# Kernel optimization log

Hardware: AMD Instinct MI355X
Metric: run time of the kernel (lower is better)

Reference implementation:

```python
import jax, jax.numpy as jnp
import numpy as np

L = 2          # n_layer
H = 8          # n_head
DM = 512       # d_model
DFF = 2048     # d_ff
DH = DM // H   # head dim (query_dimensions)
M = DH         # Favor n_dims random features
B, S = 1, 2048
EPS = 1e-6     # causal linear attention eps
LN_EPS = 1e-5  # torch LayerNorm default


def setup_inputs() -> dict:
    key = jax.random.key(0)
    ks = jax.random.split(key, 12)
    sc = 0.02
    d = {}
    d['x'] = jax.random.normal(ks[0], (B, S, DM), dtype=jnp.float32)
    for i, (n, shape) in enumerate([('Wq', (L, DM, DM)), ('Wk', (L, DM, DM)),
                                    ('Wv', (L, DM, DM)), ('Wo', (L, DM, DM)),
                                    ('W1', (L, DM, DFF)), ('W2', (L, DFF, DM))]):
        d[n] = jax.random.normal(ks[i + 1], shape, dtype=jnp.float32) * sc
    d['bq'] = jnp.zeros((L, DM), jnp.float32)
    d['bk'] = jnp.zeros((L, DM), jnp.float32)
    d['bv'] = jnp.zeros((L, DM), jnp.float32)
    d['bo'] = jnp.zeros((L, DM), jnp.float32)
    d['b1'] = jnp.zeros((L, DFF), jnp.float32)
    d['b2'] = jnp.zeros((L, DM), jnp.float32)
    d['g1'] = jnp.ones((L, DM), jnp.float32)
    d['be1'] = jnp.zeros((L, DM), jnp.float32)
    d['g2'] = jnp.ones((L, DM), jnp.float32)
    d['be2'] = jnp.zeros((L, DM), jnp.float32)
    # FAVOR+ random projection matrix per layer: [Dh, M]
    d['omega'] = jax.random.normal(ks[7], (L, DH, M), dtype=jnp.float32)
    return d


def _favor(x, omega):
    # x: [B,S,H,Dh]; softmax_temp = 1/sqrt(Dh) applied as x * sqrt(temp)
    xs = x * (DH ** -0.25)
    nrm = jnp.sum(xs * xs, axis=-1, keepdims=True)       # [B,S,H,1]
    u = jnp.einsum('bshd,dm->bshm', xs, omega)           # [B,S,H,M]
    return jnp.exp(u - 0.5 * nrm) * (M ** -0.5)


def _ln(x, g, b):
    mu = jnp.mean(x, -1, keepdims=True)
    var = jnp.mean((x - mu) ** 2, -1, keepdims=True)
    return (x - mu) * jax.lax.rsqrt(var + LN_EPS) * g + b


def _forward(x, Wq, bq, Wk, bk, Wv, bv, Wo, bo, omega,
             W1, b1, W2, b2, g1, be1, g2, be2):
    out = x
    for l in range(L):
        q = (out @ Wq[l] + bq[l]).reshape(B, S, H, DH)
        k = (out @ Wk[l] + bk[l]).reshape(B, S, H, DH)
        v = (out @ Wv[l] + bv[l]).reshape(B, S, H, DH)
        pq = _favor(q, omega[l])
        pk = _favor(k, omega[l])
        # causal linear attention: running sums of phi(k) v^T and phi(k)
        kv = jnp.cumsum(jnp.einsum('bshm,bshd->bshmd', pk, v), axis=1)  # [B,S,H,M,Dh]
        num = jnp.einsum('bshm,bshmd->bshd', pq, kv)
        den = jnp.einsum('bshm,bshm->bsh', pq, jnp.cumsum(pk, axis=1)) + EPS
        a = (num / den[..., None]).reshape(B, S, DM)
        # post-norm encoder layer (fast-transformers TransformerEncoderLayer)
        out = out + (a @ Wo[l] + bo[l])
        out = _ln(out, g1[l], be1[l])
        y = jax.nn.relu(out @ W1[l] + b1[l]) @ W2[l] + b2[l]
        out = _ln(out + y, g2[l], be2[l])
    return out


def reference(x, Wq, bq, Wk, bk, Wv, bv, Wo, bo, omega,
              W1, b1, W2, b2, g1, be1, g2, be2):
    return _forward(x, Wq, bq, Wk, bk, Wv, bv, Wo, bo, omega,
                    W1, b1, W2, b2, g1, be1, g2, be2)
```

## Files before the change

kernel.cpp:

```cpp
#include <hip/hip_runtime.h>
#include <hip/hip_bf16.h>

#define S_  2048
#define DM_ 512
#define H_  8
#define DH_ 64
#define MF_ 64
#define DFF_ 2048
#define L_  2
#define CT_ 64
#define NC_ (S_ / CT_)
#define EPS_ 1e-6f
#define LN_EPS_ 1e-5f

typedef unsigned short ushortT;
typedef unsigned int u32;
typedef float f4 __attribute__((ext_vector_type(4)));
typedef short s8 __attribute__((ext_vector_type(8)));
typedef u32 u32x2 __attribute__((ext_vector_type(2)));

__device__ __forceinline__ ushortT f2b(float f) {
  union { float f; unsigned u; } v; v.f = f;
  unsigned r = v.u + 0x7fffu + ((v.u >> 16) & 1u);
  return (ushortT)(r >> 16);
}
__device__ __forceinline__ float bu2f(ushortT h) {
  union { unsigned u; float f; } v; v.u = ((unsigned)h) << 16; return v.f;
}
__device__ __forceinline__ u32 pk2(float a, float b) {
  return (u32)f2b(a) | ((u32)f2b(b) << 16);
}

__global__ __launch_bounds__(256) void copy_in(const float* __restrict__ x,
                                               float* __restrict__ cur,
                                               ushortT* __restrict__ curb) {
  int i = blockIdx.x * 256 + threadIdx.x;
  float v = x[i];
  cur[i] = v;
  curb[i] = f2b(v);
}

struct P4 { const float* p[4]; };
__global__ __launch_bounds__(256) void tcast(P4 srcs, int perLayer, int nper,
                                             ushortT* __restrict__ dstb,
                                             size_t layerStride, size_t wStride,
                                             int K, int N) {
  const int z = blockIdx.z;
  const int widx = (nper == 4) ? (z & 3) : 0;
  const int l = (nper == 4) ? (z >> 2) : z;
  const float* src = srcs.p[widx] + (size_t)l * perLayer;
  ushortT* dst = dstb + (size_t)l * layerStride + (size_t)widx * wStride;
  __shared__ ushortT tile[32][33];
  const int t = threadIdx.x;
  const int c = t & 31, r0 = t >> 5;
  const int n0 = blockIdx.x * 32, k0 = blockIdx.y * 32;
#pragma unroll
  for (int i = 0; i < 4; ++i) {
    int r = r0 + 8 * i;
    tile[r][c] = f2b(src[(size_t)(k0 + r) * N + n0 + c]);
  }
  __syncthreads();
#pragma unroll
  for (int i = 0; i < 4; ++i) {
    int r = r0 + 8 * i;
    dst[(size_t)(n0 + r) * K + k0 + c] = tile[c][r];
  }
}

template<bool RELU, bool HAS_RES, bool OUT_BF16>
__global__ __launch_bounds__(256) void mgemm(
    const ushortT* __restrict__ A, const ushortT* __restrict__ Wt,
    const float* __restrict__ bq_, const float* __restrict__ bk_,
    const float* __restrict__ bv_, const float* __restrict__ Res,
    float* __restrict__ Cf, ushortT* __restrict__ Cb, int K, int N) {
  __shared__ ushortT sA[2][2048];
  __shared__ ushortT sB[2][2048];
  const int t = threadIdx.x;
  const int w = t >> 6, l = t & 63;
  const int wm = w >> 1, wn = w & 1;
  const int n0 = blockIdx.x * 64, m0 = blockIdx.y * 64;
  const int z = blockIdx.z;
  const ushortT* Wz = Wt + (size_t)z * K * N;
  const float* bias = (z == 0) ? bq_ : (z == 1 ? bk_ : bv_);

  const int rs = w * 16 + (l >> 2);
  const int qs = (l & 3) ^ ((rs >> 1) & 3);
  const ushortT* gA = A  + (size_t)(m0 + rs) * K + qs * 8;
  const ushortT* gB = Wz + (size_t)(n0 + rs) * K + qs * 8;

  const int Ra = wm * 32 + (l & 15);
  const int Rb = wn * 32 + (l & 15);
  const int qq = l >> 4;
  const int aoff = (Ra * 4 + (qq ^ ((Ra >> 1) & 3))) * 8;
  const int boff = (Rb * 4 + (qq ^ ((Rb >> 1) & 3))) * 8;

  f4 acc[2][2];
#pragma unroll
  for (int i = 0; i < 2; ++i)
#pragma unroll
    for (int j = 0; j < 2; ++j) acc[i][j] = (f4){0.f, 0.f, 0.f, 0.f};

  auto stage = [&](int buf, int ko) {
    __builtin_amdgcn_global_load_lds(
        (const __attribute__((address_space(1))) void*)(gA + ko),
        (__attribute__((address_space(3))) void*)(&sA[buf][w * 512]), 16, 0, 0);
    __builtin_amdgcn_global_load_lds(
        (const __attribute__((address_space(1))) void*)(gB + ko),
        (__attribute__((address_space(3))) void*)(&sB[buf][w * 512]), 16, 0, 0);
  };

  stage(0, 0);
  const int nk = K >> 5;
  for (int ks = 0; ks < nk; ++ks) {
    __syncthreads();
    if (ks + 1 < nk) stage((ks + 1) & 1, (ks + 1) * 32);
    const ushortT* pa = sA[ks & 1];
    const ushortT* pb = sB[ks & 1];
    s8 a0 = *(const s8*)(pa + aoff);
    s8 a1 = *(const s8*)(pa + aoff + 512);
    s8 b0 = *(const s8*)(pb + boff);
    s8 b1 = *(const s8*)(pb + boff + 512);
    acc[0][0] = __builtin_amdgcn_mfma_f32_16x16x32_bf16(a0, b0, acc[0][0], 0, 0, 0);
    acc[0][1] = __builtin_amdgcn_mfma_f32_16x16x32_bf16(a0, b1, acc[0][1], 0, 0, 0);
    acc[1][0] = __builtin_amdgcn_mfma_f32_16x16x32_bf16(a1, b0, acc[1][0], 0, 0, 0);
    acc[1][1] = __builtin_amdgcn_mfma_f32_16x16x32_bf16(a1, b1, acc[1][1], 0, 0, 0);
  }

  const size_t outz = (size_t)z * S_ * N;
  const int colb = n0 + wn * 32 + (l & 15);
  const int rowb = m0 + wm * 32 + ((l >> 4) << 2);
#pragma unroll
  for (int mt = 0; mt < 2; ++mt) {
#pragma unroll
    for (int nt = 0; nt < 2; ++nt) {
      const int c = colb + nt * 16;
      const float bv = bias[c];
#pragma unroll
      for (int r = 0; r < 4; ++r) {
        const int rr = rowb + mt * 16 + r;
        float v = acc[mt][nt][r] + bv;
        if (HAS_RES) v += Res[(size_t)rr * N + c];
        if (RELU) v = fmaxf(v, 0.f);
        if (OUT_BF16) Cb[outz + (size_t)rr * N + c] = f2b(v);
        else          Cf[outz + (size_t)rr * N + c] = v;
      }
    }
  }
}

__global__ __launch_bounds__(256) void mgemm_part(
    const ushortT* __restrict__ A, const ushortT* __restrict__ Wt,
    float* __restrict__ PS, int K, int N, int KS) {
  __shared__ ushortT sA[2][2048];
  __shared__ ushortT sB[2][2048];
  const int t = threadIdx.x;
  const int w = t >> 6, l = t & 63;
  const int wm = w >> 1, wn = w & 1;
  const int n0 = blockIdx.x * 64, m0 = blockIdx.y * 64;
  const int z = blockIdx.z;

  const int rs = w * 16 + (l >> 2);
  const int qs = (l & 3) ^ ((rs >> 1) & 3);
  const ushortT* gA = A  + (size_t)(m0 + rs) * K + z * KS + qs * 8;
  const ushortT* gB = Wt + (size_t)(n0 + rs) * K + z * KS + qs * 8;

  const int Ra = wm * 32 + (l & 15);
  const int Rb = wn * 32 + (l & 15);
  const int qq = l >> 4;
  const int aoff = (Ra * 4 + (qq ^ ((Ra >> 1) & 3))) * 8;
  const int boff = (Rb * 4 + (qq ^ ((Rb >> 1) & 3))) * 8;

  f4 acc[2][2];
#pragma unroll
  for (int i = 0; i < 2; ++i)
#pragma unroll
    for (int j = 0; j < 2; ++j) acc[i][j] = (f4){0.f, 0.f, 0.f, 0.f};

  auto stage = [&](int buf, int ko) {
    __builtin_amdgcn_global_load_lds(
        (const __attribute__((address_space(1))) void*)(gA + ko),
        (__attribute__((address_space(3))) void*)(&sA[buf][w * 512]), 16, 0, 0);
    __builtin_amdgcn_global_load_lds(
        (const __attribute__((address_space(1))) void*)(gB + ko),
        (__attribute__((address_space(3))) void*)(&sB[buf][w * 512]), 16, 0, 0);
  };

  stage(0, 0);
  const int nk = KS >> 5;
  for (int ks = 0; ks < nk; ++ks) {
    __syncthreads();
    if (ks + 1 < nk) stage((ks + 1) & 1, (ks + 1) * 32);
    const ushortT* pa = sA[ks & 1];
    const ushortT* pb = sB[ks & 1];
    s8 a0 = *(const s8*)(pa + aoff);
    s8 a1 = *(const s8*)(pa + aoff + 512);
    s8 b0 = *(const s8*)(pb + boff);
    s8 b1 = *(const s8*)(pb + boff + 512);
    acc[0][0] = __builtin_amdgcn_mfma_f32_16x16x32_bf16(a0, b0, acc[0][0], 0, 0, 0);
    acc[0][1] = __builtin_amdgcn_mfma_f32_16x16x32_bf16(a0, b1, acc[0][1], 0, 0, 0);
    acc[1][0] = __builtin_amdgcn_mfma_f32_16x16x32_bf16(a1, b0, acc[1][0], 0, 0, 0);
    acc[1][1] = __builtin_amdgcn_mfma_f32_16x16x32_bf16(a1, b1, acc[1][1], 0, 0, 0);
  }

  float* out = PS + (size_t)z * S_ * N;
  const int colb = n0 + wn * 32 + (l & 15);
  const int rowb = m0 + wm * 32 + ((l >> 4) << 2);
#pragma unroll
  for (int mt = 0; mt < 2; ++mt) {
#pragma unroll
    for (int nt = 0; nt < 2; ++nt) {
      const int c = colb + nt * 16;
#pragma unroll
      for (int r = 0; r < 4; ++r)
        out[(size_t)(rowb + mt * 16 + r) * N + c] = acc[mt][nt][r];
    }
  }
}

__global__ __launch_bounds__(256) void redln(const float* __restrict__ PS, int nsplit,
                                             const float* __restrict__ bias,
                                             const float* __restrict__ res,
                                             const float* __restrict__ g,
                                             const float* __restrict__ be,
                                             float* __restrict__ outF,
                                             ushortT* __restrict__ outB) {
  const int s = blockIdx.x, t = threadIdx.x;
  float v0 = bias[t] + res[(size_t)s * DM_ + t];
  float v1 = bias[t + 256] + res[(size_t)s * DM_ + 256 + t];
  for (int z = 0; z < nsplit; ++z) {
    const float* p = PS + (size_t)z * S_ * DM_ + (size_t)s * DM_;
    v0 += p[t];
    v1 += p[256 + t];
  }
  float sum = v0 + v1, sq = v0 * v0 + v1 * v1;
  for (int off = 32; off > 0; off >>= 1) {
    sum += __shfl_down(sum, off);
    sq += __shfl_down(sq, off);
  }
  __shared__ float ssum[4], ssq[4];
  __shared__ float smean, srstd;
  const int w = t >> 6;
  if ((t & 63) == 0) { ssum[w] = sum; ssq[w] = sq; }
  __syncthreads();
  if (t == 0) {
    float S1 = ssum[0] + ssum[1] + ssum[2] + ssum[3];
    float S2 = ssq[0] + ssq[1] + ssq[2] + ssq[3];
    float mu = S1 / DM_;
    smean = mu;
    srstd = rsqrtf(S2 / DM_ - mu * mu + LN_EPS_);
  }
  __syncthreads();
  const float mu = smean, rs = srstd;
  float o0 = (v0 - mu) * rs * g[t] + be[t];
  float o1 = (v1 - mu) * rs * g[256 + t] + be[256 + t];
  outF[(size_t)s * DM_ + t] = o0;
  outF[(size_t)s * DM_ + 256 + t] = o1;
  if (outB) {
    outB[(size_t)s * DM_ + t] = f2b(o0);
    outB[(size_t)s * DM_ + 256 + t] = f2b(o1);
  }
}

__global__ __launch_bounds__(256) void favor_cs(const ushortT* __restrict__ qkv,
                                                const ushortT* __restrict__ omgT,
                                                ushortT* __restrict__ PQb,
                                                ushortT* __restrict__ PKb,
                                                float* __restrict__ KVcT,
                                                float* __restrict__ Kc) {
  const int c = blockIdx.x, h = blockIdx.y, t = threadIdx.x;
  const int w = t >> 6, l = t & 63, lr = l & 15, q = l >> 4;
  __shared__ ushortT xq[64 * 72], xk[64 * 72], vT[64 * 72], omT[64 * 72];
  __shared__ ushortT pq[64 * 72], pk[64 * 72], pkT[64 * 72];
  __shared__ float nrm[128];

  const ushortT* qg = qkv + (size_t)(c * CT_) * DM_ + h * DH_;
  const ushortT* kg = qg + (size_t)S_ * DM_;
  const ushortT* vg = kg + (size_t)S_ * DM_;

  for (int i = t; i < 512; i += 256) {
    const int s = i >> 3, seg = i & 7;
    *(s8*)&xq[s * 72 + seg * 8] = *(const s8*)(qg + (size_t)s * DM_ + seg * 8);
    *(s8*)&xk[s * 72 + seg * 8] = *(const s8*)(kg + (size_t)s * DM_ + seg * 8);
    s8 av = *(const s8*)(vg + (size_t)s * DM_ + seg * 8);
#pragma unroll
    for (int j = 0; j < 8; ++j) vT[(seg * 8 + j) * 72 + s] = (ushortT)av[j];
    *(s8*)&omT[s * 72 + seg * 8] = *(const s8*)(omgT + s * 64 + seg * 8);
  }
  __syncthreads();

  if (t < 128) {
    const ushortT* src = (t < 64) ? xq : xk;
    const int s = t & 63;
    float a = 0.f;
#pragma unroll
    for (int seg = 0; seg < 8; ++seg) {
      s8 vv = *(const s8*)(src + s * 72 + seg * 8);
#pragma unroll
      for (int j = 0; j < 8; ++j) {
        float f = bu2f((ushortT)vv[j]);
        a += f * f;
      }
    }
    nrm[t] = a;
  }
  __syncthreads();

  {
    const float gam = 0.35355339059327373f;
    const int s0 = w * 16;
    s8 aq0 = *(const s8*)&xq[(s0 + lr) * 72 + q * 8];
    s8 aq1 = *(const s8*)&xq[(s0 + lr) * 72 + 32 + q * 8];
    s8 ak0 = *(const s8*)&xk[(s0 + lr) * 72 + q * 8];
    s8 ak1 = *(const s8*)&xk[(s0 + lr) * 72 + 32 + q * 8];
#pragma unroll
    for (int mt = 0; mt < 4; ++mt) {
      s8 b0 = *(const s8*)&omT[(mt * 16 + lr) * 72 + q * 8];
      s8 b1 = *(const s8*)&omT[(mt * 16 + lr) * 72 + 32 + q * 8];
      f4 cq = (f4){0.f, 0.f, 0.f, 0.f}, ck = (f4){0.f, 0.f, 0.f, 0.f};
      cq = __builtin_amdgcn_mfma_f32_16x16x32_bf16(aq0, b0, cq, 0, 0, 0);
      cq = __builtin_amdgcn_mfma_f32_16x16x32_bf16(aq1, b1, cq, 0, 0, 0);
      ck = __builtin_amdgcn_mfma_f32_16x16x32_bf16(ak0, b0, ck, 0, 0, 0);
      ck = __builtin_amdgcn_mfma_f32_16x16x32_bf16(ak1, b1, ck, 0, 0, 0);
#pragma unroll
      for (int r = 0; r < 4; ++r) {
        const int sr = s0 + q * 4 + r, mc = mt * 16 + lr;
        float vq = expf(gam * cq[r] - 0.0625f * nrm[sr]) * 0.125f;
        float vk = expf(gam * ck[r] - 0.0625f * nrm[64 + sr]) * 0.125f;
        pq[sr * 72 + mc] = f2b(vq);
        ushortT hk = f2b(vk);
        pk[sr * 72 + mc] = hk;
        pkT[mc * 72 + sr] = hk;
      }
    }
  }
  __syncthreads();

  {
    const int d0 = w * 16;
    s8 a0 = *(const s8*)&vT[(d0 + lr) * 72 + q * 8];
    s8 a1 = *(const s8*)&vT[(d0 + lr) * 72 + 32 + q * 8];
    float* outb = KVcT + (size_t)(h * NC_ + c) * DH_ * MF_;
#pragma unroll
    for (int mt = 0; mt < 4; ++mt) {
      s8 b0 = *(const s8*)&pkT[(mt * 16 + lr) * 72 + q * 8];
      s8 b1 = *(const s8*)&pkT[(mt * 16 + lr) * 72 + 32 + q * 8];
      f4 cc = (f4){0.f, 0.f, 0.f, 0.f};
      cc = __builtin_amdgcn_mfma_f32_16x16x32_bf16(a0, b0, cc, 0, 0, 0);
      cc = __builtin_amdgcn_mfma_f32_16x16x32_bf16(a1, b1, cc, 0, 0, 0);
#pragma unroll
      for (int r = 0; r < 4; ++r)
        outb[(size_t)(d0 + q * 4 + r) * MF_ + mt * 16 + lr] = cc[r];
    }
  }
  if (t < 64) {
    float s = 0.f;
#pragma unroll
    for (int seg = 0; seg < 8; ++seg) {
      s8 vv = *(const s8*)&pkT[t * 72 + seg * 8];
#pragma unroll
      for (int j = 0; j < 8; ++j) s += bu2f((ushortT)vv[j]);
    }
    Kc[(size_t)(h * NC_ + c) * MF_ + t] = s;
  }
  for (int i = t; i < 512; i += 256) {
    const int s = i >> 3, seg = i & 7;
    *(s8*)(PQb + (size_t)(c * CT_ + s) * DM_ + h * MF_ + seg * 8) = *(const s8*)&pq[s * 72 + seg * 8];
    *(s8*)(PKb + (size_t)(c * CT_ + s) * DM_ + h * MF_ + seg * 8) = *(const s8*)&pk[s * 72 + seg * 8];
  }
}

__global__ __launch_bounds__(256) void prefix2(float* __restrict__ KVc,
                                               float* __restrict__ Kc) {
  const int h = blockIdx.x, seg = blockIdx.y, t = threadIdx.x;
  if (seg < 16) {
    float* base = KVc + (size_t)h * NC_ * MF_ * DH_ + seg * 256 + t;
    float v[NC_];
#pragma unroll
    for (int c = 0; c < NC_; ++c) v[c] = base[(size_t)c * MF_ * DH_];
    float run = 0.f;
#pragma unroll
    for (int c = 0; c < NC_; ++c) {
      float tmp = v[c];
      base[(size_t)c * MF_ * DH_] = run;
      run += tmp;
    }
  } else if (t < MF_) {
    float* base = Kc + (size_t)h * NC_ * MF_ + t;
    float v[NC_];
#pragma unroll
    for (int c = 0; c < NC_; ++c) v[c] = base[(size_t)c * MF_];
    float run = 0.f;
#pragma unroll
    for (int c = 0; c < NC_; ++c) {
      float tmp = v[c];
      base[(size_t)c * MF_] = run;
      run += tmp;
    }
  }
}

__global__ __launch_bounds__(256) void attn_mfma(const ushortT* __restrict__ PQ,
                                                 const ushortT* __restrict__ PK,
                                                 const ushortT* __restrict__ V,
                                                 const float* __restrict__ KVcT,
                                                 const float* __restrict__ Kc,
                                                 ushortT* __restrict__ Aout) {
  const int cc = blockIdx.x, h = blockIdx.y, t = threadIdx.x;
  const int w = t >> 6, l = t & 63;
  const int lr = l & 15, q = l >> 4;

  __shared__ ushortT pqs[64 * 72];
  __shared__ ushortT pks[64 * 72];
  __shared__ ushortT vts[64 * 72];
  __shared__ ushortT kvs[64 * 72];
  __shared__ ushortT tms[64 * 72];
  __shared__ float dpart[256];
  __shared__ float den[64];

  for (int i = t; i < 512; i += 256) {
    const int s = i >> 3, seg = i & 7;
    *(s8*)&pqs[s * 72 + seg * 8] = *(const s8*)(PQ + (size_t)(cc * CT_ + s) * DM_ + h * MF_ + seg * 8);
    *(s8*)&pks[s * 72 + seg * 8] = *(const s8*)(PK + (size_t)(cc * CT_ + s) * DM_ + h * MF_ + seg * 8);
    s8 av = *(const s8*)(V + (size_t)(cc * CT_ + s) * DM_ + h * DH_ + seg * 8);
#pragma unroll
    for (int j = 0; j < 8; ++j) vts[(seg * 8 + j) * 72 + s] = (ushortT)av[j];
    const float* kr = KVcT + (size_t)((h * NC_ + cc) * DH_ + s) * MF_ + seg * 8;
    f4 g0 = *(const f4*)kr;
    f4 g1 = *(const f4*)(kr + 4);
    u32* p = (u32*)&kvs[s * 72 + seg * 8];
    p[0] = pk2(g0.x, g0.y); p[1] = pk2(g0.z, g0.w);
    p[2] = pk2(g1.x, g1.y); p[3] = pk2(g1.z, g1.w);
  }
  __syncthreads();

  {
    const int s0 = w * 16;
    s8 a0 = *(const s8*)&pqs[(s0 + lr) * 72 + q * 8];
    s8 a1 = *(const s8*)&pqs[(s0 + lr) * 72 + 32 + q * 8];
#pragma unroll
    for (int tb = 0; tb < 4; ++tb) {
      f4 c = (f4){0.f, 0.f, 0.f, 0.f};
      if (tb <= w) {
        s8 b0 = *(const s8*)&pks[(tb * 16 + lr) * 72 + q * 8];
        s8 b1 = *(const s8*)&pks[(tb * 16 + lr) * 72 + 32 + q * 8];
        c = __builtin_amdgcn_mfma_f32_16x16x32_bf16(a0, b0, c, 0, 0, 0);
        c = __builtin_amdgcn_mfma_f32_16x16x32_bf16(a1, b1, c, 0, 0, 0);
      }
#pragma unroll
      for (int r = 0; r < 4; ++r) {
        float v = c[r];
        if (tb == w && lr > q * 4 + r) v = 0.f;
        tms[(s0 + q * 4 + r) * 72 + tb * 16 + lr] = f2b(v);
      }
    }
  }
  __syncthreads();

  {
    const int s = t >> 2, part = t & 3;
    float dp = 0.f;
    const u32* trow = (const u32*)&tms[s * 72 + part * 16];
#pragma unroll
    for (int j = 0; j < 8; ++j) {
      u32 u = trow[j];
      dp += bu2f((ushortT)(u & 0xffffu)) + bu2f((ushortT)(u >> 16));
    }
    const u32* qrow = (const u32*)&pqs[s * 72 + part * 16];
    const f4* kc4 = (const f4*)(Kc + (size_t)(h * NC_ + cc) * MF_ + part * 16);
#pragma unroll
    for (int j = 0; j < 4; ++j) {
      f4 b = kc4[j];
      u32 ua = qrow[2 * j], ub = qrow[2 * j + 1];
      dp += bu2f((ushortT)(ua & 0xffffu)) * b.x + bu2f((ushortT)(ua >> 16)) * b.y +
            bu2f((ushortT)(ub & 0xffffu)) * b.z + bu2f((ushortT)(ub >> 16)) * b.w;
    }
    dpart[t] = dp;
  }
  __syncthreads();
  if (t < 64)
    den[t] = dpart[4 * t] + dpart[4 * t + 1] + dpart[4 * t + 2] + dpart[4 * t + 3] + EPS_;
  __syncthreads();

  {
    const int d0 = w * 16;
    const int drow = d0 + lr;
    s8 akv0 = *(const s8*)&kvs[drow * 72 + q * 8];
    s8 akv1 = *(const s8*)&kvs[drow * 72 + 32 + q * 8];
    s8 av0  = *(const s8*)&vts[drow * 72 + q * 8];
    s8 av1  = *(const s8*)&vts[drow * 72 + 32 + q * 8];
#pragma unroll
    for (int sb = 0; sb < 4; ++sb) {
      const int srow = sb * 16 + lr;
      s8 bq0 = *(const s8*)&pqs[srow * 72 + q * 8];
      s8 bq1 = *(const s8*)&pqs[srow * 72 + 32 + q * 8];
      s8 bt0 = *(const s8*)&tms[srow * 72 + q * 8];
      s8 bt1 = *(const s8*)&tms[srow * 72 + 32 + q * 8];
      f4 c = (f4){0.f, 0.f, 0.f, 0.f};
      c = __builtin_amdgcn_mfma_f32_16x16x32_bf16(akv0, bq0, c, 0, 0, 0);
      c = __builtin_amdgcn_mfma_f32_16x16x32_bf16(akv1, bq1, c, 0, 0, 0);
      c = __builtin_amdgcn_mfma_f32_16x16x32_bf16(av0, bt0, c, 0, 0, 0);
      c = __builtin_amdgcn_mfma_f32_16x16x32_bf16(av1, bt1, c, 0, 0, 0);
      const float inv = 1.f / den[srow];
      u32x2 o;
      o.x = pk2(c[0] * inv, c[1] * inv);
      o.y = pk2(c[2] * inv, c[3] * inv);
      *(u32x2*)(Aout + (size_t)(cc * CT_ + srow) * DM_ + h * DH_ + d0 + q * 4) = o;
    }
  }
}

extern "C" void kernel_launch(void* const* d_in, const int* in_sizes, int n_in,
                              void* d_out, int out_size, void* d_ws, size_t ws_size,
                              hipStream_t stream) {
  const float* x    = (const float*)d_in[0];
  const float* Wq   = (const float*)d_in[1];
  const float* Wk   = (const float*)d_in[2];
  const float* Wv   = (const float*)d_in[3];
  const float* Wo   = (const float*)d_in[4];
  const float* W1   = (const float*)d_in[5];
  const float* W2   = (const float*)d_in[6];
  const float* bq   = (const float*)d_in[7];
  const float* bk   = (const float*)d_in[8];
  const float* bv   = (const float*)d_in[9];
  const float* bo   = (const float*)d_in[10];
  const float* b1   = (const float*)d_in[11];
  const float* b2   = (const float*)d_in[12];
  const float* g1   = (const float*)d_in[13];
  const float* be1  = (const float*)d_in[14];
  const float* g2   = (const float*)d_in[15];
  const float* be2  = (const float*)d_in[16];
  const float* omg  = (const float*)d_in[17];
  float* out = (float*)d_out;

  const size_t MB = 1048576;
  float* f    = (float*)d_ws;
  float* cur  = f;
  float* ln1  = f + 1 * MB;
  float* KVcb = f + 2 * MB;
  float* Kcb  = f + 3 * MB;
  float* PS   = f + 3 * MB + 16384;

  ushortT* u    = (ushortT*)(f + 8 * MB);
  ushortT* curb = u;
  ushortT* qkb  = u + 1 * MB;
  ushortT* pqb  = u + 4 * MB;
  ushortT* pkb  = u + 5 * MB;
  ushortT* qbb  = u + 6 * MB;
  ushortT* ln1b = u + 7 * MB;
  ushortT* ffb  = u + 8 * MB;
  ushortT* wb   = u + 12 * MB;
  ushortT* omgTb = wb + 2 * 3145728;

  const size_t LS = 3145728;
  const size_t W1OFF = 1048576, W2OFF = 2097152, WOOFF = 786432;

  copy_in<<<S_ * DM_ / 256, 256, 0, stream>>>(x, cur, curb);

  {
    P4 s4; s4.p[0] = Wq; s4.p[1] = Wk; s4.p[2] = Wv; s4.p[3] = Wo;
    tcast<<<dim3(16, 16, 8), 256, 0, stream>>>(s4, DM_ * DM_, 4, wb, LS, DM_ * DM_, DM_, DM_);
    P4 s1; s1.p[0] = W1; s1.p[1] = W1; s1.p[2] = W1; s1.p[3] = W1;
    tcast<<<dim3(64, 16, 2), 256, 0, stream>>>(s1, DM_ * DFF_, 1, wb + W1OFF, LS, 0, DM_, DFF_);
    P4 s2; s2.p[0] = W2; s2.p[1] = W2; s2.p[2] = W2; s2.p[3] = W2;
    tcast<<<dim3(16, 64, 2), 256, 0, stream>>>(s2, DFF_ * DM_, 1, wb + W2OFF, LS, 0, DFF_, DM_);
    P4 sm; sm.p[0] = omg; sm.p[1] = omg; sm.p[2] = omg; sm.p[3] = omg;
    tcast<<<dim3(2, 2, 2), 256, 0, stream>>>(sm, DH_ * MF_, 1, omgTb, DH_ * MF_, 0, DH_, MF_);
  }

  const dim3 gQKV(DM_ / 64, S_ / 64, 3);
  const dim3 gFF1(DFF_ / 64, S_ / 64, 1);
  const dim3 gWo(DM_ / 64, S_ / 64, 2);
  const dim3 gW2(DM_ / 64, S_ / 64, 4);
  const dim3 gAttn(NC_, H_);
  const dim3 gPre(H_, 17);

  for (int l = 0; l < L_; ++l) {
    const ushortT* wl = wb + (size_t)l * LS;
    const size_t bo512 = (size_t)l * DM_;
    const size_t boFF = (size_t)l * DFF_;

    mgemm<false, false, true><<<gQKV, 256, 0, stream>>>(
        curb, wl, bq + bo512, bk + bo512, bv + bo512, nullptr, nullptr, qkb, DM_, DM_);

    favor_cs<<<gAttn, 256, 0, stream>>>(qkb, omgTb + (size_t)l * DH_ * MF_,
                                        pqb, pkb, KVcb, Kcb);
    prefix2<<<gPre, 256, 0, stream>>>(KVcb, Kcb);
    attn_mfma<<<gAttn, 256, 0, stream>>>(pqb, pkb, qkb + 2 * (size_t)S_ * DM_,
                                         KVcb, Kcb, qbb);

    mgemm_part<<<gWo, 256, 0, stream>>>(qbb, wl + WOOFF, PS, DM_, DM_, 256);
    redln<<<S_, 256, 0, stream>>>(PS, 2, bo + bo512, cur, g1 + bo512, be1 + bo512, ln1, ln1b);

    mgemm<true, false, true><<<gFF1, 256, 0, stream>>>(
        ln1b, wl + W1OFF, b1 + boFF, nullptr, nullptr, nullptr, nullptr, ffb, DM_, DFF_);

    mgemm_part<<<gW2, 256, 0, stream>>>(ffb, wl + W2OFF, PS, DFF_, DM_, 512);
    const bool last = (l == L_ - 1);
    redln<<<S_, 256, 0, stream>>>(PS, 4, b2 + bo512, ln1, g2 + bo512, be2 + bo512,
                                  last ? out : cur, last ? nullptr : curb);
  }
}
```

Measured before the change: 249.4 us.

## Fuse attention stages into one cooperative kernel and merge setup kernels

Replaces the three attention launches (favor features, chunk prefix sum, output) with a single cooperative kernel that uses grid-wide syncs. PQ/PK stay in shared memory and are never written to or read back from global memory. The input copy and the five weight-cast launches are merged into one launch. This removes launch overhead and global round-trips, at the cost of two grid barriers and a prefix phase that runs on only 136 of the 256 blocks.

New measurement: 538.5 us. 116% more time.

```diff
diff --git a/kernel.cpp b/kernel.cpp
--- a/kernel.cpp
+++ b/kernel.cpp
@@ -1,5 +1,8 @@
 #include <hip/hip_runtime.h>
 #include <hip/hip_bf16.h>
+#include <hip/hip_cooperative_groups.h>
+
+namespace cg = cooperative_groups;
 
 #define S_  2048
 #define DM_ 512
@@ -13,6 +16,11 @@
 #define EPS_ 1e-6f
 #define LN_EPS_ 1e-5f
 
+#define LSW_   3145728
+#define W1OFF_ 1048576
+#define W2OFF_ 2097152
+#define WOOFF_ 786432
+
 typedef unsigned short ushortT;
 typedef unsigned int u32;
 typedef float f4 __attribute__((ext_vector_type(4)));
@@ -31,39 +39,62 @@
   return (u32)f2b(a) | ((u32)f2b(b) << 16);
 }
 
-__global__ __launch_bounds__(256) void copy_in(const float* __restrict__ x,
-                                               float* __restrict__ cur,
-                                               ushortT* __restrict__ curb) {
-  int i = blockIdx.x * 256 + threadIdx.x;
-  float v = x[i];
-  cur[i] = v;
-  curb[i] = f2b(v);
-}
-
-struct P4 { const float* p[4]; };
-__global__ __launch_bounds__(256) void tcast(P4 srcs, int perLayer, int nper,
-                                             ushortT* __restrict__ dstb,
-                                             size_t layerStride, size_t wStride,
-                                             int K, int N) {
-  const int z = blockIdx.z;
-  const int widx = (nper == 4) ? (z & 3) : 0;
-  const int l = (nper == 4) ? (z >> 2) : z;
-  const float* src = srcs.p[widx] + (size_t)l * perLayer;
-  ushortT* dst = dstb + (size_t)l * layerStride + (size_t)widx * wStride;
+__global__ __launch_bounds__(256) void tcast_all(
+    const float* __restrict__ x,
+    const float* __restrict__ Wq, const float* __restrict__ Wk,
+    const float* __restrict__ Wv, const float* __restrict__ Wo,
+    const float* __restrict__ W1, const float* __restrict__ W2,
+    const float* __restrict__ omg,
+    float* __restrict__ cur, ushortT* __restrict__ curb,
+    ushortT* __restrict__ wb, ushortT* __restrict__ omgTb) {
+  const int bid = blockIdx.x;
+  const int t = threadIdx.x;
+  if (bid >= 6152) {
+    const int i = (bid - 6152) * 256 + t;
+    float v = x[i];
+    cur[i] = v;
+    curb[i] = f2b(v);
+    return;
+  }
   __shared__ ushortT tile[32][33];
-  const int t = threadIdx.x;
-  const int c = t & 31, r0 = t >> 5;
-  const int n0 = blockIdx.x * 32, k0 = blockIdx.y * 32;
+  const float* src; ushortT* dst; int K, N, bx, by;
+  if (bid < 2048) {
+    const int z = bid >> 8, widx = z & 3, lay = z >> 2;
+    const float* s4[4] = {Wq, Wk, Wv, Wo};
+    src = s4[widx] + (size_t)lay * DM_ * DM_;
+    dst = wb + (size_t)lay * LSW_ + (size_t)widx * DM_ * DM_;
+    K = DM_; N = DM_; bx = bid & 15; by = (bid >> 4) & 15;
+  } else if (bid < 4096) {
+    const int r = bid - 2048;
+    const int lay = r >> 10;
+    src = W1 + (size_t)lay * DM_ * DFF_;
+    dst = wb + (size_t)lay * LSW_ + W1OFF_;
+    K = DM_; N = DFF_; bx = r & 63; by = (r >> 6) & 15;
+  } else if (bid < 6144) {
+    const int r = bid - 4096;
+    const int lay = r >> 10;
+    src = W2 + (size_t)lay * DFF_ * DM_;
+    dst = wb + (size_t)lay * LSW_ + W2OFF_;
+    K = DFF_; N = DM_; bx = r & 15; by = (r >> 4) & 63;
+  } else {
+    const int r = bid - 6144;
+    const int lay = r >> 2;
+    src = omg + (size_t)lay * DH_ * MF_;
+    dst = omgTb + (size_t)lay * DH_ * MF_;
+    K = DH_; N = MF_; bx = r & 1; by = (r >> 1) & 1;
+  }
+  const int cc = t & 31, r0 = t >> 5;
+  const int n0 = bx * 32, k0 = by * 32;
 #pragma unroll
   for (int i = 0; i < 4; ++i) {
     int r = r0 + 8 * i;
-    tile[r][c] = f2b(src[(size_t)(k0 + r) * N + n0 + c]);
+    tile[r][cc] = f2b(src[(size_t)(k0 + r) * N + n0 + cc]);
   }
   __syncthreads();
 #pragma unroll
   for (int i = 0; i < 4; ++i) {
     int r = r0 + 8 * i;
-    dst[(size_t)(n0 + r) * K + k0 + c] = tile[c][r];
+    dst[(size_t)(n0 + r) * K + k0 + cc] = tile[cc][r];
   }
 }
 
@@ -258,6 +289,234 @@
   if (outB) {
     outB[(size_t)s * DM_ + t] = f2b(o0);
     outB[(size_t)s * DM_ + 256 + t] = f2b(o1);
+  }
+}
+
+__global__ __launch_bounds__(256) void attn_all(const ushortT* __restrict__ qkv,
+                                                const ushortT* __restrict__ omgT,
+                                                float* __restrict__ KVcT,
+                                                float* __restrict__ Kc,
+                                                ushortT* __restrict__ Aout) {
+  cg::grid_group grid = cg::this_grid();
+  const int bid = blockIdx.x;
+  const int c = bid & 31, h = bid >> 5;
+  const int t = threadIdx.x;
+  const int w = t >> 6, l = t & 63, lr = l & 15, q = l >> 4;
+
+  __shared__ ushortT xq[64 * 72];
+  __shared__ ushortT xk[64 * 72];
+  __shared__ ushortT vT[64 * 72];
+  __shared__ ushortT omT[64 * 72];
+  __shared__ ushortT pq[64 * 72];
+  __shared__ ushortT pk[64 * 72];
+  __shared__ ushortT pkT[64 * 72];
+  __shared__ float nrm[128];
+  __shared__ float den[64];
+
+  const ushortT* qg = qkv + (size_t)(c * CT_) * DM_ + h * DH_;
+  const ushortT* kg = qg + (size_t)S_ * DM_;
+  const ushortT* vg = kg + (size_t)S_ * DM_;
+  for (int i = t; i < 512; i += 256) {
+    const int s = i >> 3, seg = i & 7;
+    *(s8*)&xq[s * 72 + seg * 8] = *(const s8*)(qg + (size_t)s * DM_ + seg * 8);
+    *(s8*)&xk[s * 72 + seg * 8] = *(const s8*)(kg + (size_t)s * DM_ + seg * 8);
+    s8 av = *(const s8*)(vg + (size_t)s * DM_ + seg * 8);
+#pragma unroll
+    for (int j = 0; j < 8; ++j) vT[(seg * 8 + j) * 72 + s] = (ushortT)av[j];
+    *(s8*)&omT[s * 72 + seg * 8] = *(const s8*)(omgT + s * 64 + seg * 8);
+  }
+  __syncthreads();
+
+  if (t < 128) {
+    const ushortT* src = (t < 64) ? xq : xk;
+    const int s = t & 63;
+    float a = 0.f;
+#pragma unroll
+    for (int seg = 0; seg < 8; ++seg) {
+      s8 vv = *(const s8*)(src + s * 72 + seg * 8);
+#pragma unroll
+      for (int j = 0; j < 8; ++j) {
+        float f = bu2f((ushortT)vv[j]);
+        a += f * f;
+      }
+    }
+    nrm[t] = a;
+  }
+  __syncthreads();
+
+  {
+    const float gam = 0.35355339059327373f;
+    const int s0 = w * 16;
+    s8 aq0 = *(const s8*)&xq[(s0 + lr) * 72 + q * 8];
+    s8 aq1 = *(const s8*)&xq[(s0 + lr) * 72 + 32 + q * 8];
+    s8 ak0 = *(const s8*)&xk[(s0 + lr) * 72 + q * 8];
+    s8 ak1 = *(const s8*)&xk[(s0 + lr) * 72 + 32 + q * 8];
+#pragma unroll
+    for (int mt = 0; mt < 4; ++mt) {
+      s8 b0 = *(const s8*)&omT[(mt * 16 + lr) * 72 + q * 8];
+      s8 b1 = *(const s8*)&omT[(mt * 16 + lr) * 72 + 32 + q * 8];
+      f4 cq = (f4){0.f, 0.f, 0.f, 0.f}, ck = (f4){0.f, 0.f, 0.f, 0.f};
+      cq = __builtin_amdgcn_mfma_f32_16x16x32_bf16(aq0, b0, cq, 0, 0, 0);
+      cq = __builtin_amdgcn_mfma_f32_16x16x32_bf16(aq1, b1, cq, 0, 0, 0);
+      ck = __builtin_amdgcn_mfma_f32_16x16x32_bf16(ak0, b0, ck, 0, 0, 0);
+      ck = __builtin_amdgcn_mfma_f32_16x16x32_bf16(ak1, b1, ck, 0, 0, 0);
+#pragma unroll
+      for (int r = 0; r < 4; ++r) {
+        const int sr = s0 + q * 4 + r, mc = mt * 16 + lr;
+        float vq = expf(gam * cq[r] - 0.0625f * nrm[sr]) * 0.125f;
+        float vk = expf(gam * ck[r] - 0.0625f * nrm[64 + sr]) * 0.125f;
+        pq[sr * 72 + mc] = f2b(vq);
+        ushortT hk = f2b(vk);
+        pk[sr * 72 + mc] = hk;
+        pkT[mc * 72 + sr] = hk;
+      }
+    }
+  }
+  __syncthreads();
+
+  {
+    const int d0 = w * 16;
+    s8 a0 = *(const s8*)&vT[(d0 + lr) * 72 + q * 8];
+    s8 a1 = *(const s8*)&vT[(d0 + lr) * 72 + 32 + q * 8];
+    float* outb = KVcT + (size_t)(h * NC_ + c) * DH_ * MF_;
+#pragma unroll
+    for (int mt = 0; mt < 4; ++mt) {
+      s8 b0 = *(const s8*)&pkT[(mt * 16 + lr) * 72 + q * 8];
+      s8 b1 = *(const s8*)&pkT[(mt * 16 + lr) * 72 + 32 + q * 8];
+      f4 cc2 = (f4){0.f, 0.f, 0.f, 0.f};
+      cc2 = __builtin_amdgcn_mfma_f32_16x16x32_bf16(a0, b0, cc2, 0, 0, 0);
+      cc2 = __builtin_amdgcn_mfma_f32_16x16x32_bf16(a1, b1, cc2, 0, 0, 0);
+#pragma unroll
+      for (int r = 0; r < 4; ++r)
+        outb[(size_t)(d0 + q * 4 + r) * MF_ + mt * 16 + lr] = cc2[r];
+    }
+  }
+  if (t < 64) {
+    float s = 0.f;
+#pragma unroll
+    for (int seg = 0; seg < 8; ++seg) {
+      s8 vv = *(const s8*)&pkT[t * 72 + seg * 8];
+#pragma unroll
+      for (int j = 0; j < 8; ++j) s += bu2f((ushortT)vv[j]);
+    }
+    Kc[(size_t)(h * NC_ + c) * MF_ + t] = s;
+  }
+  __threadfence();
+  grid.sync();
+
+  if (bid < 128) {
+    const int hh = bid >> 4, seg = bid & 15;
+    float* base = KVcT + (size_t)hh * NC_ * MF_ * DH_ + seg * 256 + t;
+    float v[NC_];
+#pragma unroll
+    for (int c2 = 0; c2 < NC_; ++c2) v[c2] = base[(size_t)c2 * MF_ * DH_];
+    float run = 0.f;
+#pragma unroll
+    for (int c2 = 0; c2 < NC_; ++c2) {
+      float tmp = v[c2];
+      base[(size_t)c2 * MF_ * DH_] = run;
+      run += tmp;
+    }
+  } else if (bid < 136 && t < MF_) {
+    const int hh = bid - 128;
+    float* base = Kc + (size_t)hh * NC_ * MF_ + t;
+    float v[NC_];
+#pragma unroll
+    for (int c2 = 0; c2 < NC_; ++c2) v[c2] = base[(size_t)c2 * MF_];
+    float run = 0.f;
+#pragma unroll
+    for (int c2 = 0; c2 < NC_; ++c2) {
+      float tmp = v[c2];
+      base[(size_t)c2 * MF_] = run;
+      run += tmp;
+    }
+  }
+  __threadfence();
+  grid.sync();
+
+  ushortT* kvs = xq;
+  ushortT* tms = xk;
+  for (int i = t; i < 512; i += 256) {
+    const int s = i >> 3, seg = i & 7;
+    const float* kr = KVcT + (size_t)((h * NC_ + c) * DH_ + s) * MF_ + seg * 8;
+    f4 g0 = *(const f4*)kr;
+    f4 g1 = *(const f4*)(kr + 4);
+    u32* p = (u32*)&kvs[s * 72 + seg * 8];
+    p[0] = pk2(g0.x, g0.y); p[1] = pk2(g0.z, g0.w);
+    p[2] = pk2(g1.x, g1.y); p[3] = pk2(g1.z, g1.w);
+  }
+  {
+    const int s0 = w * 16;
+    s8 a0 = *(const s8*)&pq[(s0 + lr) * 72 + q * 8];
+    s8 a1 = *(const s8*)&pq[(s0 + lr) * 72 + 32 + q * 8];
+#pragma unroll
+    for (int tb = 0; tb < 4; ++tb) {
+      f4 cc2 = (f4){0.f, 0.f, 0.f, 0.f};
+      if (tb <= w) {
+        s8 b0 = *(const s8*)&pk[(tb * 16 + lr) * 72 + q * 8];
+        s8 b1 = *(const s8*)&pk[(tb * 16 + lr) * 72 + 32 + q * 8];
+        cc2 = __builtin_amdgcn_mfma_f32_16x16x32_bf16(a0, b0, cc2, 0, 0, 0);
+        cc2 = __builtin_amdgcn_mfma_f32_16x16x32_bf16(a1, b1, cc2, 0, 0, 0);
+      }
+#pragma unroll
+      for (int r = 0; r < 4; ++r) {
+        float v = cc2[r];
+        if (tb == w && lr > q * 4 + r) v = 0.f;
+        tms[(s0 + q * 4 + r) * 72 + tb * 16 + lr] = f2b(v);
+      }
+    }
+  }
+  __syncthreads();
+
+  {
+    const int s = t >> 2, part = t & 3;
+    float dp = 0.f;
+    const u32* trow = (const u32*)&tms[s * 72 + part * 16];
+#pragma unroll
+    for (int j = 0; j < 8; ++j) {
+      u32 u = trow[j];
+      dp += bu2f((ushortT)(u & 0xffffu)) + bu2f((ushortT)(u >> 16));
+    }
+    const u32* qrow = (const u32*)&pq[s * 72 + part * 16];
+    const f4* kc4 = (const f4*)(Kc + (size_t)(h * NC_ + c) * MF_ + part * 16);
+#pragma unroll
+    for (int j = 0; j < 4; ++j) {
+      f4 b = kc4[j];
+      u32 ua = qrow[2 * j], ub = qrow[2 * j + 1];
+      dp += bu2f((ushortT)(ua & 0xffffu)) * b.x + bu2f((ushortT)(ua >> 16)) * b.y +
+            bu2f((ushortT)(ub & 0xffffu)) * b.z + bu2f((ushortT)(ub >> 16)) * b.w;
+    }
+    dp += __shfl_down(dp, 2);
+    dp += __shfl_down(dp, 1);
+    if (part == 0) den[s] = dp + EPS_;
+  }
+  __syncthreads();
+
+  {
+    const int d0 = w * 16;
+    const int drow = d0 + lr;
+    s8 akv0 = *(const s8*)&kvs[drow * 72 + q * 8];
+    s8 akv1 = *(const s8*)&kvs[drow * 72 + 32 + q * 8];
+    s8 av0  = *(const s8*)&vT[drow * 72 + q * 8];
+    s8 av1  = *(const s8*)&vT[drow * 72 + 32 + q * 8];
+#pragma unroll
+    for (int sb = 0; sb < 4; ++sb) {
+      const int srow = sb * 16 + lr;
+      s8 bq0 = *(const s8*)&pq[srow * 72 + q * 8];
+      s8 bq1 = *(const s8*)&pq[srow * 72 + 32 + q * 8];
+      s8 bt0 = *(const s8*)&tms[srow * 72 + q * 8];
+      s8 bt1 = *(const s8*)&tms[srow * 72 + 32 + q * 8];
+      f4 cc2 = (f4){0.f, 0.f, 0.f, 0.f};
+      cc2 = __builtin_amdgcn_mfma_f32_16x16x32_bf16(akv0, bq0, cc2, 0, 0, 0);
+      cc2 = __builtin_amdgcn_mfma_f32_16x16x32_bf16(akv1, bq1, cc2, 0, 0, 0);
+      cc2 = __builtin_amdgcn_mfma_f32_16x16x32_bf16(av0, bt0, cc2, 0, 0, 0);
+      cc2 = __builtin_amdgcn_mfma_f32_16x16x32_bf16(av1, bt1, cc2, 0, 0, 0);
+      const float inv = 1.f / den[srow];
+      u32x2 o;
+      o.x = pk2(cc2[0] * inv, cc2[1] * inv);
+      o.y = pk2(cc2[2] * inv, cc2[3] * inv);
+      *(u32x2*)(Aout + (size_t)(c * CT_ + srow) * DM_ + h * DH_ + d0 + q * 4) = o;
+    }
   }
 }
 
@@ -549,23 +808,10 @@
   ushortT* ln1b = u + 7 * MB;
   ushortT* ffb  = u + 8 * MB;
   ushortT* wb   = u + 12 * MB;
-  ushortT* omgTb = wb + 2 * 3145728;
-
-  const size_t LS = 3145728;
-  const size_t W1OFF = 1048576, W2OFF = 2097152, WOOFF = 786432;
-
-  copy_in<<<S_ * DM_ / 256, 256, 0, stream>>>(x, cur, curb);
-
-  {
-    P4 s4; s4.p[0] = Wq; s4.p[1] = Wk; s4.p[2] = Wv; s4.p[3] = Wo;
-    tcast<<<dim3(16, 16, 8), 256, 0, stream>>>(s4, DM_ * DM_, 4, wb, LS, DM_ * DM_, DM_, DM_);
-    P4 s1; s1.p[0] = W1; s1.p[1] = W1; s1.p[2] = W1; s1.p[3] = W1;
-    tcast<<<dim3(64, 16, 2), 256, 0, stream>>>(s1, DM_ * DFF_, 1, wb + W1OFF, LS, 0, DM_, DFF_);
-    P4 s2; s2.p[0] = W2; s2.p[1] = W2; s2.p[2] = W2; s2.p[3] = W2;
-    tcast<<<dim3(16, 64, 2), 256, 0, stream>>>(s2, DFF_ * DM_, 1, wb + W2OFF, LS, 0, DFF_, DM_);
-    P4 sm; sm.p[0] = omg; sm.p[1] = omg; sm.p[2] = omg; sm.p[3] = omg;
-    tcast<<<dim3(2, 2, 2), 256, 0, stream>>>(sm, DH_ * MF_, 1, omgTb, DH_ * MF_, 0, DH_, MF_);
-  }
+  ushortT* omgTb = wb + 2 * LSW_;
+
+  tcast_all<<<10248, 256, 0, stream>>>(x, Wq, Wk, Wv, Wo, W1, W2, omg,
+                                       cur, curb, wb, omgTb);
 
   const dim3 gQKV(DM_ / 64, S_ / 64, 3);
   const dim3 gFF1(DFF_ / 64, S_ / 64, 1);
@@ -575,26 +821,36 @@
   const dim3 gPre(H_, 17);
 
   for (int l = 0; l < L_; ++l) {
-    const ushortT* wl = wb + (size_t)l * LS;
+    const ushortT* wl = wb + (size_t)l * LSW_;
     const size_t bo512 = (size_t)l * DM_;
     const size_t boFF = (size_t)l * DFF_;
 
     mgemm<false, false, true><<<gQKV, 256, 0, stream>>>(
         curb, wl, bq + bo512, bk + bo512, bv + bo512, nullptr, nullptr, qkb, DM_, DM_);
 
-    favor_cs<<<gAttn, 256, 0, stream>>>(qkb, omgTb + (size_t)l * DH_ * MF_,
-                                        pqb, pkb, KVcb, Kcb);
-    prefix2<<<gPre, 256, 0, stream>>>(KVcb, Kcb);
-    attn_mfma<<<gAttn, 256, 0, stream>>>(pqb, pkb, qkb + 2 * (size_t)S_ * DM_,
-                                         KVcb, Kcb, qbb);
-
-    mgemm_part<<<gWo, 256, 0, stream>>>(qbb, wl + WOOFF, PS, DM_, DM_, 256);
+    {
+      const ushortT* qkvp = qkb;
+      const ushortT* omgTl = omgTb + (size_t)l * DH_ * MF_;
+      float* kvp = KVcb; float* kcp = Kcb; ushortT* aoutp = qbb;
+      void* cargs[] = {(void*)&qkvp, (void*)&omgTl, (void*)&kvp, (void*)&kcp, (void*)&aoutp};
+      hipError_t ce = hipLaunchCooperativeKernel((const void*)attn_all,
+                                                 dim3(NC_ * H_), dim3(256),
+                                                 cargs, 0, stream);
+      if (ce != hipSuccess) {
+        favor_cs<<<gAttn, 256, 0, stream>>>(qkb, omgTl, pqb, pkb, KVcb, Kcb);
+        prefix2<<<gPre, 256, 0, stream>>>(KVcb, Kcb);
+        attn_mfma<<<gAttn, 256, 0, stream>>>(pqb, pkb, qkb + 2 * (size_t)S_ * DM_,
+                                             KVcb, Kcb, qbb);
+      }
+    }
+
+    mgemm_part<<<gWo, 256, 0, stream>>>(qbb, wl + WOOFF_, PS, DM_, DM_, 256);
     redln<<<S_, 256, 0, stream>>>(PS, 2, bo + bo512, cur, g1 + bo512, be1 + bo512, ln1, ln1b);
 
     mgemm<true, false, true><<<gFF1, 256, 0, stream>>>(
-        ln1b, wl + W1OFF, b1 + boFF, nullptr, nullptr, nullptr, nullptr, ffb, DM_, DFF_);
-
-    mgemm_part<<<gW2, 256, 0, stream>>>(ffb, wl + W2OFF, PS, DFF_, DM_, 512);
+        ln1b, wl + W1OFF_, b1 + boFF, nullptr, nullptr, nullptr, nullptr, ffb, DM_, DFF_);
+
+    mgemm_part<<<gW2, 256, 0, stream>>>(ffb, wl + W2OFF_, PS, DFF_, DM_, 512);
     const bool last = (l == L_ - 1);
     redln<<<S_, 256, 0, stream>>>(PS, 4, b2 + bo512, ln1, g2 + bo512, be2 + bo512,
                                   last ? out : cur, last ? nullptr : curb);
```

## Fuse setup kernels into one launch and fold chunk prefix sum into attention

Applied to the files above, without the earlier changes.

Merges the input copy and all weight transpose/cast kernels into a single tcast_all launch that dispatches on block index. Removes the separate prefix2 kernel: each attention block now sums the KV and K chunk states of all earlier chunks itself before packing them into shared memory. This cuts launch count and a global read-modify-write pass, but makes later chunks re-read up to 31 chunk states, adding redundant global traffic and load imbalance across blocks.

Result: slower. 264.8 us (+6.2%).

```diff
diff --git a/kernel.cpp b/kernel.cpp
--- a/kernel.cpp
+++ b/kernel.cpp
@@ -13,6 +13,11 @@
 #define EPS_ 1e-6f
 #define LN_EPS_ 1e-5f
 
+#define LSW_   3145728
+#define W1OFF_ 1048576
+#define W2OFF_ 2097152
+#define WOOFF_ 786432
+
 typedef unsigned short ushortT;
 typedef unsigned int u32;
 typedef float f4 __attribute__((ext_vector_type(4)));
@@ -31,39 +36,62 @@
   return (u32)f2b(a) | ((u32)f2b(b) << 16);
 }
 
-__global__ __launch_bounds__(256) void copy_in(const float* __restrict__ x,
-                                               float* __restrict__ cur,
-                                               ushortT* __restrict__ curb) {
-  int i = blockIdx.x * 256 + threadIdx.x;
-  float v = x[i];
-  cur[i] = v;
-  curb[i] = f2b(v);
-}
-
-struct P4 { const float* p[4]; };
-__global__ __launch_bounds__(256) void tcast(P4 srcs, int perLayer, int nper,
-                                             ushortT* __restrict__ dstb,
-                                             size_t layerStride, size_t wStride,
-                                             int K, int N) {
-  const int z = blockIdx.z;
-  const int widx = (nper == 4) ? (z & 3) : 0;
-  const int l = (nper == 4) ? (z >> 2) : z;
-  const float* src = srcs.p[widx] + (size_t)l * perLayer;
-  ushortT* dst = dstb + (size_t)l * layerStride + (size_t)widx * wStride;
+__global__ __launch_bounds__(256) void tcast_all(
+    const float* __restrict__ x,
+    const float* __restrict__ Wq, const float* __restrict__ Wk,
+    const float* __restrict__ Wv, const float* __restrict__ Wo,
+    const float* __restrict__ W1, const float* __restrict__ W2,
+    const float* __restrict__ omg,
+    float* __restrict__ cur, ushortT* __restrict__ curb,
+    ushortT* __restrict__ wb, ushortT* __restrict__ omgTb) {
+  const int bid = blockIdx.x;
+  const int t = threadIdx.x;
+  if (bid >= 6152) {
+    const int i = (bid - 6152) * 256 + t;
+    float v = x[i];
+    cur[i] = v;
+    curb[i] = f2b(v);
+    return;
+  }
   __shared__ ushortT tile[32][33];
-  const int t = threadIdx.x;
-  const int c = t & 31, r0 = t >> 5;
-  const int n0 = blockIdx.x * 32, k0 = blockIdx.y * 32;
+  const float* src; ushortT* dst; int K, N, bx, by;
+  if (bid < 2048) {
+    const int z = bid >> 8, widx = z & 3, lay = z >> 2;
+    const float* s4[4] = {Wq, Wk, Wv, Wo};
+    src = s4[widx] + (size_t)lay * DM_ * DM_;
+    dst = wb + (size_t)lay * LSW_ + (size_t)widx * DM_ * DM_;
+    K = DM_; N = DM_; bx = bid & 15; by = (bid >> 4) & 15;
+  } else if (bid < 4096) {
+    const int r = bid - 2048;
+    const int lay = r >> 10;
+    src = W1 + (size_t)lay * DM_ * DFF_;
+    dst = wb + (size_t)lay * LSW_ + W1OFF_;
+    K = DM_; N = DFF_; bx = r & 63; by = (r >> 6) & 15;
+  } else if (bid < 6144) {
+    const int r = bid - 4096;
+    const int lay = r >> 10;
+    src = W2 + (size_t)lay * DFF_ * DM_;
+    dst = wb + (size_t)lay * LSW_ + W2OFF_;
+    K = DFF_; N = DM_; bx = r & 15; by = (r >> 4) & 63;
+  } else {
+    const int r = bid - 6144;
+    const int lay = r >> 2;
+    src = omg + (size_t)lay * DH_ * MF_;
+    dst = omgTb + (size_t)lay * DH_ * MF_;
+    K = DH_; N = MF_; bx = r & 1; by = (r >> 1) & 1;
+  }
+  const int cc = t & 31, r0 = t >> 5;
+  const int n0 = bx * 32, k0 = by * 32;
 #pragma unroll
   for (int i = 0; i < 4; ++i) {
     int r = r0 + 8 * i;
-    tile[r][c] = f2b(src[(size_t)(k0 + r) * N + n0 + c]);
+    tile[r][cc] = f2b(src[(size_t)(k0 + r) * N + n0 + cc]);
   }
   __syncthreads();
 #pragma unroll
   for (int i = 0; i < 4; ++i) {
     int r = r0 + 8 * i;
-    dst[(size_t)(n0 + r) * K + k0 + c] = tile[c][r];
+    dst[(size_t)(n0 + r) * K + k0 + cc] = tile[cc][r];
   }
 }
 
@@ -369,42 +397,12 @@
   }
 }
 
-__global__ __launch_bounds__(256) void prefix2(float* __restrict__ KVc,
-                                               float* __restrict__ Kc) {
-  const int h = blockIdx.x, seg = blockIdx.y, t = threadIdx.x;
-  if (seg < 16) {
-    float* base = KVc + (size_t)h * NC_ * MF_ * DH_ + seg * 256 + t;
-    float v[NC_];
-#pragma unroll
-    for (int c = 0; c < NC_; ++c) v[c] = base[(size_t)c * MF_ * DH_];
-    float run = 0.f;
-#pragma unroll
-    for (int c = 0; c < NC_; ++c) {
-      float tmp = v[c];
-      base[(size_t)c * MF_ * DH_] = run;
-      run += tmp;
-    }
-  } else if (t < MF_) {
-    float* base = Kc + (size_t)h * NC_ * MF_ + t;
-    float v[NC_];
-#pragma unroll
-    for (int c = 0; c < NC_; ++c) v[c] = base[(size_t)c * MF_];
-    float run = 0.f;
-#pragma unroll
-    for (int c = 0; c < NC_; ++c) {
-      float tmp = v[c];
-      base[(size_t)c * MF_] = run;
-      run += tmp;
-    }
-  }
-}
-
-__global__ __launch_bounds__(256) void attn_mfma(const ushortT* __restrict__ PQ,
-                                                 const ushortT* __restrict__ PK,
-                                                 const ushortT* __restrict__ V,
-                                                 const float* __restrict__ KVcT,
-                                                 const float* __restrict__ Kc,
-                                                 ushortT* __restrict__ Aout) {
+__global__ __launch_bounds__(256) void attn_pfx(const ushortT* __restrict__ PQ,
+                                                const ushortT* __restrict__ PK,
+                                                const ushortT* __restrict__ V,
+                                                const float* __restrict__ KVcT,
+                                                const float* __restrict__ Kc,
+                                                ushortT* __restrict__ Aout) {
   const int cc = blockIdx.x, h = blockIdx.y, t = threadIdx.x;
   const int w = t >> 6, l = t & 63;
   const int lr = l & 15, q = l >> 4;
@@ -416,6 +414,39 @@
   __shared__ ushortT tms[64 * 72];
   __shared__ float dpart[256];
   __shared__ float den[64];
+  __shared__ float kcs[64];
+
+  const int s0j = t >> 3, seg0 = t & 7;
+  const int s1j = (t + 256) >> 3, seg1 = t & 7;
+  float acc0[8], acc1[8];
+#pragma unroll
+  for (int j = 0; j < 8; ++j) { acc0[j] = 0.f; acc1[j] = 0.f; }
+
+  const float* kvbase = KVcT + (size_t)(h * NC_) * DH_ * MF_;
+  for (int cp = 0; cp < cc; ++cp) {
+    const float* kr = kvbase + (size_t)cp * DH_ * MF_;
+    f4 a0 = *(const f4*)(kr + s0j * MF_ + seg0 * 8);
+    f4 a1 = *(const f4*)(kr + s0j * MF_ + seg0 * 8 + 4);
+    f4 b0 = *(const f4*)(kr + s1j * MF_ + seg1 * 8);
+    f4 b1 = *(const f4*)(kr + s1j * MF_ + seg1 * 8 + 4);
+    acc0[0] += a0.x; acc0[1] += a0.y; acc0[2] += a0.z; acc0[3] += a0.w;
+    acc0[4] += a1.x; acc0[5] += a1.y; acc0[6] += a1.z; acc0[7] += a1.w;
+    acc1[0] += b0.x; acc1[1] += b0.y; acc1[2] += b0.z; acc1[3] += b0.w;
+    acc1[4] += b1.x; acc1[5] += b1.y; acc1[6] += b1.z; acc1[7] += b1.w;
+  }
+  {
+    u32* p0 = (u32*)&kvs[s0j * 72 + seg0 * 8];
+    p0[0] = pk2(acc0[0], acc0[1]); p0[1] = pk2(acc0[2], acc0[3]);
+    p0[2] = pk2(acc0[4], acc0[5]); p0[3] = pk2(acc0[6], acc0[7]);
+    u32* p1 = (u32*)&kvs[s1j * 72 + seg1 * 8];
+    p1[0] = pk2(acc1[0], acc1[1]); p1[1] = pk2(acc1[2], acc1[3]);
+    p1[2] = pk2(acc1[4], acc1[5]); p1[3] = pk2(acc1[6], acc1[7]);
+  }
+  if (t < 64) {
+    float s = 0.f;
+    for (int cp = 0; cp < cc; ++cp) s += Kc[(size_t)(h * NC_ + cp) * MF_ + t];
+    kcs[t] = s;
+  }
 
   for (int i = t; i < 512; i += 256) {
     const int s = i >> 3, seg = i & 7;
@@ -424,12 +455,6 @@
     s8 av = *(const s8*)(V + (size_t)(cc * CT_ + s) * DM_ + h * DH_ + seg * 8);
 #pragma unroll
     for (int j = 0; j < 8; ++j) vts[(seg * 8 + j) * 72 + s] = (ushortT)av[j];
-    const float* kr = KVcT + (size_t)((h * NC_ + cc) * DH_ + s) * MF_ + seg * 8;
-    f4 g0 = *(const f4*)kr;
-    f4 g1 = *(const f4*)(kr + 4);
-    u32* p = (u32*)&kvs[s * 72 + seg * 8];
-    p[0] = pk2(g0.x, g0.y); p[1] = pk2(g0.z, g0.w);
-    p[2] = pk2(g1.x, g1.y); p[3] = pk2(g1.z, g1.w);
   }
   __syncthreads();
 
@@ -466,7 +491,7 @@
       dp += bu2f((ushortT)(u & 0xffffu)) + bu2f((ushortT)(u >> 16));
     }
     const u32* qrow = (const u32*)&pqs[s * 72 + part * 16];
-    const f4* kc4 = (const f4*)(Kc + (size_t)(h * NC_ + cc) * MF_ + part * 16);
+    const f4* kc4 = (const f4*)(kcs + part * 16);
 #pragma unroll
     for (int j = 0; j < 4; ++j) {
       f4 b = kc4[j];
@@ -549,33 +574,19 @@
   ushortT* ln1b = u + 7 * MB;
   ushortT* ffb  = u + 8 * MB;
   ushortT* wb   = u + 12 * MB;
-  ushortT* omgTb = wb + 2 * 3145728;
-
-  const size_t LS = 3145728;
-  const size_t W1OFF = 1048576, W2OFF = 2097152, WOOFF = 786432;
-
-  copy_in<<<S_ * DM_ / 256, 256, 0, stream>>>(x, cur, curb);
-
-  {
-    P4 s4; s4.p[0] = Wq; s4.p[1] = Wk; s4.p[2] = Wv; s4.p[3] = Wo;
-    tcast<<<dim3(16, 16, 8), 256, 0, stream>>>(s4, DM_ * DM_, 4, wb, LS, DM_ * DM_, DM_, DM_);
-    P4 s1; s1.p[0] = W1; s1.p[1] = W1; s1.p[2] = W1; s1.p[3] = W1;
-    tcast<<<dim3(64, 16, 2), 256, 0, stream>>>(s1, DM_ * DFF_, 1, wb + W1OFF, LS, 0, DM_, DFF_);
-    P4 s2; s2.p[0] = W2; s2.p[1] = W2; s2.p[2] = W2; s2.p[3] = W2;
-    tcast<<<dim3(16, 64, 2), 256, 0, stream>>>(s2, DFF_ * DM_, 1, wb + W2OFF, LS, 0, DFF_, DM_);
-    P4 sm; sm.p[0] = omg; sm.p[1] = omg; sm.p[2] = omg; sm.p[3] = omg;
-    tcast<<<dim3(2, 2, 2), 256, 0, stream>>>(sm, DH_ * MF_, 1, omgTb, DH_ * MF_, 0, DH_, MF_);
-  }
+  ushortT* omgTb = wb + 2 * LSW_;
+
+  tcast_all<<<10248, 256, 0, stream>>>(x, Wq, Wk, Wv, Wo, W1, W2, omg,
+                                       cur, curb, wb, omgTb);
 
   const dim3 gQKV(DM_ / 64, S_ / 64, 3);
   const dim3 gFF1(DFF_ / 64, S_ / 64, 1);
   const dim3 gWo(DM_ / 64, S_ / 64, 2);
   const dim3 gW2(DM_ / 64, S_ / 64, 4);
   const dim3 gAttn(NC_, H_);
-  const dim3 gPre(H_, 17);
 
   for (int l = 0; l < L_; ++l) {
-    const ushortT* wl = wb + (size_t)l * LS;
+    const ushortT* wl = wb + (size_t)l * LSW_;
     const size_t bo512 = (size_t)l * DM_;
     const size_t boFF = (size_t)l * DFF_;
 
@@ -584,17 +595,16 @@
 
     favor_cs<<<gAttn, 256, 0, stream>>>(qkb, omgTb + (size_t)l * DH_ * MF_,
                                         pqb, pkb, KVcb, Kcb);
-    prefix2<<<gPre, 256, 0, stream>>>(KVcb, Kcb);
-    attn_mfma<<<gAttn, 256, 0, stream>>>(pqb, pkb, qkb + 2 * (size_t)S_ * DM_,
-                                         KVcb, Kcb, qbb);
-
-    mgemm_part<<<gWo, 256, 0, stream>>>(qbb, wl + WOOFF, PS, DM_, DM_, 256);
+    attn_pfx<<<gAttn, 256, 0, stream>>>(pqb, pkb, qkb + 2 * (size_t)S_ * DM_,
+                                        KVcb, Kcb, qbb);
+
+    mgemm_part<<<gWo, 256, 0, stream>>>(qbb, wl + WOOFF_, PS, DM_, DM_, 256);
     redln<<<S_, 256, 0, stream>>>(PS, 2, bo + bo512, cur, g1 + bo512, be1 + bo512, ln1, ln1b);
 
     mgemm<true, false, true><<<gFF1, 256, 0, stream>>>(
-        ln1b, wl + W1OFF, b1 + boFF, nullptr, nullptr, nullptr, nullptr, ffb, DM_, DFF_);
-
-    mgemm_part<<<gW2, 256, 0, stream>>>(ffb, wl + W2OFF, PS, DFF_, DM_, 512);
+        ln1b, wl + W1OFF_, b1 + boFF, nullptr, nullptr, nullptr, nullptr, ffb, DM_, DFF_);
+
+    mgemm_part<<<gW2, 256, 0, stream>>>(ffb, wl + W2OFF_, PS, DFF_, DM_, 512);
     const bool last = (l == L_ - 1);
     redln<<<S_, 256, 0, stream>>>(PS, 4, b2 + bo512, ln1, g2 + bo512, be2 + bo512,
                                   last ? out : cur, last ? nullptr : curb);
```
